# Performance work log

Measured on AMD Instinct MI355X. Metric: run time of the kernel, lower is better.

The kernel has to match this reference:

```python
import jax, jax.numpy as jnp
import numpy as np

PAD_Y = 16
PAD_X = 16


def setup_inputs() -> dict:
    key = jax.random.key(0)
    k1, k2, k3, k4 = jax.random.split(key, 4)
    B, NLAM, H, W = 4, 96, 256, 256
    KS = 15
    cube = jax.random.normal(k1, (B, NLAM, H, W), dtype=jnp.float32)
    # per-(ksequence, wavelength) dispersion shifts in pixels (a few px)
    dx = 3.0 * jax.random.normal(k2, (4, NLAM), dtype=jnp.float32)
    dy = 3.0 * jax.random.normal(k3, (4, NLAM), dtype=jnp.float32)
    psf = jax.random.uniform(k4, (KS, KS), dtype=jnp.float32)
    psf = psf / psf.sum()  # normalised PSF as in the original
    return {"cube": cube, "dx": dx, "dy": dy, "psf_kernel": psf}


def _forward(cube, dx, dy, psf_kernel):
    B, n_lam, H, W = cube.shape
    H_out, W_out = H + 2 * PAD_Y, W + 2 * PAD_X
    padded = jnp.pad(cube, ((0, 0), (0, 0), (PAD_Y, PAD_Y), (PAD_X, PAD_X)))
    yy, xx = jnp.meshgrid(jnp.arange(H_out, dtype=cube.dtype),
                          jnp.arange(W_out, dtype=cube.dtype), indexing="ij")

    def shift_one(img_b, d_x, d_y):
        # img_b: (B, H_out, W_out); output[y,x] = input[y-dy, x-dx], bilinear,
        # zeros outside (matches grid_sample padding_mode='zeros', align_corners=True)
        coords = jnp.stack([yy - d_y, xx - d_x])  # (2, H_out, W_out)
        return jax.vmap(lambda im: jax.scipy.ndimage.map_coordinates(
            im, coords, order=1, mode="constant", cval=0.0))(img_b)

    def per_k(dxk, dyk):
        # vmap over wavelengths -> (n_lam, B, H_out, W_out); accumulate over lambda
        shifted = jax.vmap(shift_one, in_axes=(1, 0, 0))(padded, dxk, dyk)
        return shifted.sum(0)  # (B, H_out, W_out)

    acc = jax.vmap(per_k)(dx, dy)            # (4, B, H_out, W_out)
    acc = jnp.transpose(acc, (1, 0, 2, 3))   # (B, 4, H_out, W_out)

    # PSF conv (same kernel every channel); conv is linear so conv(sum) == sum(conv)
    ks = psf_kernel.shape[-1]
    p = ks // 2
    x = acc.reshape(B * 4, 1, H_out, W_out)
    kern = psf_kernel.reshape(1, 1, ks, ks)
    out = jax.lax.conv_general_dilated(
        x, kern, window_strides=(1, 1), padding=[(p, p), (p, p)],
        dimension_numbers=("NCHW", "OIHW", "NCHW"))
    return out.reshape(B, 4, H_out, W_out)


def reference(cube, dx, dy, psf_kernel):
    return _forward(cube, dx, dy, psf_kernel)
```

## Files before the change

### kernel.cpp

```cpp
#include <hip/hip_runtime.h>

#define BB 4
#define NLAM 96
#define HH 256
#define WW 256
#define HO 288
#define WO 288
#define NK 4
#define KS 15
#define PADK 7

#define ACC_N ((size_t)BB * NK * HO * WO)

#define SP 104
#define NQ 7
#define TILE_Q (NQ * 256)

typedef float f4a __attribute__((ext_vector_type(4)));
typedef float f8v __attribute__((ext_vector_type(8), aligned(16)));

__global__ __launch_bounds__(384) void params_k(const float* __restrict__ dx,
                                                const float* __restrict__ dy,
                                                float4* __restrict__ pw,
                                                int2* __restrict__ po,
                                                int4* __restrict__ gmm,
                                                float* __restrict__ zp) {
    __shared__ int sox[384], soy[384];
    const int i = threadIdx.x;
    if (i < 32) zp[i] = 0.0f;
    const float sx = -dx[i] - 16.0f;
    const float sy = -dy[i] - 16.0f;
    const float fx = floorf(sx), fy = floorf(sy);
    const int ox = (int)fx, oy = (int)fy;
    po[i] = make_int2(ox, oy);
    pw[i] = make_float4(1.0f - (sx - fx), sx - fx, 1.0f - (sy - fy), sy - fy);
    sox[i] = ox; soy[i] = oy;
    __syncthreads();
    if (i < 64) {
        int mnx = sox[i], mxx = mnx, mny = soy[i], mxy = mny;
        for (int j = i + 64; j < 384; j += 64) {
            mnx = min(mnx, sox[j]); mxx = max(mxx, sox[j]);
            mny = min(mny, soy[j]); mxy = max(mxy, soy[j]);
        }
        for (int m = 32; m; m >>= 1) {
            mnx = min(mnx, __shfl_xor(mnx, m, 64));
            mxx = max(mxx, __shfl_xor(mxx, m, 64));
            mny = min(mny, __shfl_xor(mny, m, 64));
            mxy = max(mxy, __shfl_xor(mxy, m, 64));
        }
        if (i == 0) *gmm = make_int4(mnx, mxx, mny, mxy);
    }
}

#define HORW(P)                                                          \
    {                                                                    \
        f4a h0  = {vb0[P], vb0[(P)+1], vb0[(P)+2], vb0[(P)+3]};          \
        f4a h0s = {vb0[(P)+1], vb0[(P)+2], vb0[(P)+3], vb0[(P)+4]};      \
        f4a h1  = {vb1[P], vb1[(P)+1], vb1[(P)+2], vb1[(P)+3]};          \
        f4a h1s = {vb1[(P)+1], vb1[(P)+2], vb1[(P)+3], vb1[(P)+4]};      \
        a[k][0] += w.x * h0 + w.y * h0s;                                 \
        a[k][1] += w.x * h1 + w.y * h1s;                                 \
    }

__global__ __launch_bounds__(256, 2) void shift_accum(
        const float* __restrict__ cube,
        const float4* __restrict__ pw,
        const int2* __restrict__ po,
        const int4* __restrict__ gmm,
        const float* __restrict__ zp,
        float* __restrict__ part,
        int S, int chunk) {
    __shared__ __align__(16) float tile[TILE_Q * 4 + 8];
    const int zc  = blockIdx.z;
    const int b   = zc / S;
    const int c   = zc - b * S;
    const int tx0 = blockIdx.x * 64;
    const int ty0 = blockIdx.y * 32;
    const int tx  = threadIdx.x, ty = threadIdx.y;
    const int x   = tx0 + tx * 4;
    const int y   = ty0 + ty * 2;
    const int tid = ty * 16 + tx;
    const float* __restrict__ cb = cube + (size_t)b * NLAM * HH * WW;

    const int4 mm = *gmm;
    const int spanX = mm.y - mm.x;
    const int spanY = mm.w - mm.z;
    const bool lds_ok = (spanX <= 32) && (spanY <= 31);

    f4a a[NK][2];
#pragma unroll
    for (int k = 0; k < NK; ++k) { a[k][0] = (f4a)0.f; a[k][1] = (f4a)0.f; }

    const int l0 = min(NLAM, c * chunk);
    const int l1 = min(NLAM, l0 + chunk);

    if (lds_ok) {
        const int row0 = ty0 + mm.z;
        const int col0 = (tx0 + mm.x) & ~3;
        const int R    = spanY + 34;
        const int Rq   = R * 26;
        const int dx0  = tx0 - col0;
        const int tb0  = (ty * 2 - mm.z) * SP + tx * 4 + dx0;
        const int ldsq0 = tid & 192;
        const char* zpc = (const char*)zp;

        int goffB[NQ];
        int fm = 0;
        int pf = 0;
#pragma unroll
        for (int s = 0; s < NQ; ++s) {
            const int q  = tid + s * 256;
            const bool inR = q < Rq;
            const int r  = q / 26;
            const int qi = q - r * 26;
            const int gy = row0 + r;
            const int gc = col0 + qi * 4;
            const bool rowOK = (unsigned)gy < (unsigned)HH;
            const bool fullQ = inR && rowOK && gc >= 0 && gc <= WW - 4;
            const bool partQ = inR && rowOK && !fullQ && (gc + 3 >= 0) && (gc < WW);
            goffB[s] = (gy * WW + gc) * 4;
            if (fullQ) fm |= 1 << s;
            if (partQ) pf |= 1 << s;
        }

        for (int lam = l0; lam < l1; ++lam) {
            const char* __restrict__ ib = (const char*)(cb + lam * (HH * WW));
#pragma unroll
            for (int s = 0; s < NQ; ++s) {
                if (s * 256 < Rq) {
                    const char* src = ((fm >> s) & 1) ? (ib + goffB[s]) : zpc;
                    __builtin_amdgcn_global_load_lds(
                        (const __attribute__((address_space(1))) unsigned int*)src,
                        (__attribute__((address_space(3))) unsigned int*)
                            (tile + (s * 256 + ldsq0) * 4),
                        16, 0, 0);
                }
            }
            if (pf) {
                asm volatile("s_waitcnt vmcnt(0)" ::: "memory");
#pragma unroll
                for (int s = 0; s < NQ; ++s) {
                    if (pf & (1 << s)) {
                        const int q  = tid + s * 256;
                        const int r  = q / 26;
                        const int qi = q - r * 26;
                        const int gy = row0 + r;
                        const int gc = col0 + qi * 4;
                        const float* rp = (const float*)ib + gy * WW;
                        const int la = r * SP + qi * 4;
#pragma unroll
                        for (int e = 0; e < 4; ++e)
                            tile[la + e] = ((unsigned)(gc + e) < (unsigned)WW)
                                               ? rp[gc + e] : 0.0f;
                    }
                }
            }
            __syncthreads();
#pragma unroll
            for (int k = 0; k < NK; ++k) {
                const int2 o = po[k * NLAM + lam];
                const float4 w = pw[k * NLAM + lam];
                const int bidx = tb0 + o.y * SP + o.x;
                const int p = __builtin_amdgcn_readfirstlane(bidx & 3);
                const float* ta = tile + (bidx & ~3);
                const f8v R0 = *(const f8v*)ta;
                const f8v R1 = *(const f8v*)(ta + SP);
                const f8v R2 = *(const f8v*)(ta + 2 * SP);
                const f8v vb0 = w.z * R0 + w.w * R1;
                const f8v vb1 = w.z * R1 + w.w * R2;
                switch (p) {
                    case 0:  HORW(0); break;
                    case 1:  HORW(1); break;
                    case 2:  HORW(2); break;
                    default: HORW(3); break;
                }
            }
            __syncthreads();
        }
    } else {
        for (int lam = l0; lam < l1; ++lam) {
            const float* __restrict__ img = cb + lam * (HH * WW);
#pragma unroll
            for (int k = 0; k < NK; ++k) {
                const int i_ = k * NLAM + lam;
                const int2 o = po[i_]; const float4 w = pw[i_];
#pragma unroll
                for (int j = 0; j < 2; ++j) {
                    const int iy = y + j + o.y;
                    const int ix = x + o.x;
                    const int cy0 = min(max(iy, 0), HH - 1);
                    const int cy1 = min(max(iy + 1, 0), HH - 1);
                    const float my0 = ((unsigned)iy       < (unsigned)HH) ? w.z : 0.0f;
                    const float my1 = ((unsigned)(iy + 1) < (unsigned)HH) ? w.w : 0.0f;
                    const float* r0p = img + cy0 * WW;
                    const float* r1p = img + cy1 * WW;
                    float rb[5];
#pragma unroll
                    for (int cc = 0; cc < 5; ++cc) {
                        const int cx = min(max(ix + cc, 0), WW - 1);
                        const float m = ((unsigned)(ix + cc) < (unsigned)WW) ? 1.0f : 0.0f;
                        rb[cc] = m * (my0 * r0p[cx] + my1 * r1p[cx]);
                    }
                    f4a d;
                    d.x = w.x * rb[0] + w.y * rb[1];
                    d.y = w.x * rb[1] + w.y * rb[2];
                    d.z = w.x * rb[2] + w.y * rb[3];
                    d.w = w.x * rb[3] + w.y * rb[4];
                    a[k][j] += d;
                }
            }
        }
    }

    if (x < WO) {
        const size_t hw = (size_t)HO * WO;
        float* pa = part + (size_t)c * ACC_N + ((size_t)(b * NK) * HO + y) * WO + x;
#pragma unroll
        for (int k = 0; k < NK; ++k) {
            *(f4a*)(pa + (size_t)k * hw)      = a[k][0];
            *(f4a*)(pa + (size_t)k * hw + WO) = a[k][1];
        }
    }
}

template <int S>
__global__ __launch_bounds__(256) void reduce_k(float* __restrict__ part) {
    const size_t i = ((size_t)blockIdx.x * 256 + threadIdx.x) * 4;
    f4a acc = *(const f4a*)(part + i);
#pragma unroll
    for (int cc = 1; cc < S; ++cc)
        acc += *(const f4a*)(part + (size_t)cc * ACC_N + i);
    *(f4a*)(part + i) = acc;
}

#define CPX 112
#define CROWS 30
#define CTILE_N (CROWS * CPX)
#define NQC 5

__global__ __launch_bounds__(192) void conv_psf(const float* __restrict__ part,
                                                const float* __restrict__ psf,
                                                float* __restrict__ out) {
    __shared__ __align__(16) float tilec[CTILE_N + 16];
    __shared__ __align__(16) float spsf[KS][16];
    const int bk  = blockIdx.z;
    const int gx0 = blockIdx.x * 96 - 8;
    const int gy0 = blockIdx.y * 16 - PADK;
    const float* __restrict__ ap = part + (size_t)bk * HO * WO;

    const int tid = threadIdx.y * 24 + threadIdx.x;
    for (int i = tid; i < KS * 16; i += 192) {
        const int r = i >> 4, cc2 = i & 15;
        spsf[r][cc2] = (cc2 < KS) ? psf[r * KS + cc2] : 0.0f;
    }

#pragma unroll
    for (int s = 0; s < NQC; ++s) {
        const int q  = tid + s * 192;
        const bool inR = q < CROWS * 28;
        const int r  = q / 28;
        const int qi = q - r * 28;
        const int gy = gy0 + r;
        const int gx = gx0 + qi * 4;
        const bool rowOK = (unsigned)gy < (unsigned)HO;
        const int gyc = min(max(gy, 0), HO - 1);
        const int goffB = (gyc * WO + gx) * 4;
        const int laddr = inR ? (r * CPX + qi * 4) : CTILE_N;
        f4a m;
#pragma unroll
        for (int e = 0; e < 4; ++e)
            m[e] = (inR && rowOK && (unsigned)(gx + e) < (unsigned)WO) ? 1.0f : 0.0f;
        f4a v = *(const f4a*)((const char*)ap + goffB);
        *(f4a*)(tilec + laddr) = v * m;
    }
    __syncthreads();

    const int x0 = threadIdx.x * 4;
    const int y0 = threadIdx.y * 2;
    f4a o0 = (f4a)0.f, o1 = (f4a)0.f;
    f4a prev0, prev1, prev2, prev3;

#pragma unroll
    for (int rr = 0; rr < 16; ++rr) {
        const float* rp = &tilec[(y0 + rr) * CPX + x0];
        float row[20];
#pragma unroll
        for (int q = 0; q < 5; ++q) {
            f4a v = *(const f4a*)(rp + 4 * q);
            row[4 * q]     = v.x; row[4 * q + 1] = v.y;
            row[4 * q + 2] = v.z; row[4 * q + 3] = v.w;
        }

        f4a c0, c1, c2, c3;
        if (rr < 15) {
            c0 = *(const f4a*)&spsf[rr][0];
            c1 = *(const f4a*)&spsf[rr][4];
            c2 = *(const f4a*)&spsf[rr][8];
            c3 = *(const f4a*)&spsf[rr][12];
        }
        if (rr < 15) {
#pragma unroll
            for (int kx = 0; kx < KS; ++kx) {
                const float wv = (kx < 4) ? c0[kx] : (kx < 8) ? c1[kx - 4]
                               : (kx < 12) ? c2[kx - 8] : c3[kx - 12];
                f4a rv = {row[kx + 1], row[kx + 2], row[kx + 3], row[kx + 4]};
                o0 += wv * rv;
            }
        }
        if (rr >= 1) {
#pragma unroll
            for (int kx = 0; kx < KS; ++kx) {
                const float wv = (kx < 4) ? prev0[kx] : (kx < 8) ? prev1[kx - 4]
                               : (kx < 12) ? prev2[kx - 8] : prev3[kx - 12];
                f4a rv = {row[kx + 1], row[kx + 2], row[kx + 3], row[kx + 4]};
                o1 += wv * rv;
            }
        }
        prev0 = c0; prev1 = c1; prev2 = c2; prev3 = c3;
    }

    const int xo = blockIdx.x * 96 + x0;
    const int yo = blockIdx.y * 16 + y0;
    float* op = out + ((size_t)bk * HO + yo) * WO + xo;
    *(f4a*)op        = o0;
    *(f4a*)(op + WO) = o1;
}

extern "C" void kernel_launch(void* const* d_in, const int* in_sizes, int n_in,
                              void* d_out, int out_size, void* d_ws, size_t ws_size,
                              hipStream_t stream) {
    const float* cube = (const float*)d_in[0];
    const float* dx   = (const float*)d_in[1];
    const float* dy   = (const float*)d_in[2];
    const float* psf  = (const float*)d_in[3];
    float* out = (float*)d_out;

    const size_t ACCB   = ACC_N * sizeof(float);
    const size_t tables = 384 * sizeof(float4) + 384 * sizeof(int2) + sizeof(int4);

    int S = 1;
    for (int cand : {12, 8, 6, 4, 3, 2}) {
        if (ws_size >= 128 + (size_t)cand * ACCB + tables + 4096) { S = cand; break; }
    }
    const int chunk = (NLAM + S - 1) / S;

    float* zp   = (float*)d_ws;
    float* part = (float*)((char*)d_ws + 128);
    char*  tb   = (char*)part + (size_t)S * ACCB;
    float4* pw  = (float4*)tb;
    int2*   po  = (int2*)(tb + 384 * sizeof(float4));
    int4*   gmm = (int4*)(tb + 384 * sizeof(float4) + 384 * sizeof(int2));

    params_k<<<1, 384, 0, stream>>>(dx, dy, pw, po, gmm, zp);

    dim3 b1(16, 16);
    dim3 g1((WO + 63) / 64, HO / 32, BB * S);
    shift_accum<<<g1, b1, 0, stream>>>(cube, pw, po, gmm, zp, part, S, chunk);

    const int rblocks = (int)(ACC_N / 4 / 256);
    switch (S) {
        case 12: reduce_k<12><<<rblocks, 256, 0, stream>>>(part); break;
        case 8:  reduce_k<8><<<rblocks, 256, 0, stream>>>(part); break;
        case 6:  reduce_k<6><<<rblocks, 256, 0, stream>>>(part); break;
        case 4:  reduce_k<4><<<rblocks, 256, 0, stream>>>(part); break;
        case 3:  reduce_k<3><<<rblocks, 256, 0, stream>>>(part); break;
        case 2:  reduce_k<2><<<rblocks, 256, 0, stream>>>(part); break;
        default: break;
    }

    dim3 b2(24, 8);
    dim3 g2(WO / 96, HO / 16, BB * NK);
    conv_psf<<<g2, b2, 0, stream>>>(part, psf, out);
}
```

Baseline: 206.1 us.

## Replace split-lambda partial buffers and reduce kernel with float atomics

Each lambda-chunk block now atomically adds its accumulated values into a single zeroed accumulation buffer. This drops the S-way partial buffers and the separate reduce kernel, cutting the extra global write/read traffic and one launch. It adds a memset of the accumulator and 12-way atomic contention per output element using scalar unsafeAtomicAdd. The chunk count is fixed at 12 instead of depending on workspace size, and block index decoding now places the batch in the low bits.

```diff
diff --git a/kernel.cpp b/kernel.cpp
--- a/kernel.cpp
+++ b/kernel.cpp
@@ -16,6 +16,8 @@
 #define NQ 7
 #define TILE_Q (NQ * 256)
 
+#define NCH 12
+
 typedef float f4a __attribute__((ext_vector_type(4)));
 typedef float f8v __attribute__((ext_vector_type(8), aligned(16)));
 
@@ -23,11 +25,9 @@
                                                 const float* __restrict__ dy,
                                                 float4* __restrict__ pw,
                                                 int2* __restrict__ po,
-                                                int4* __restrict__ gmm,
-                                                float* __restrict__ zp) {
+                                                int4* __restrict__ gmm) {
     __shared__ int sox[384], soy[384];
     const int i = threadIdx.x;
-    if (i < 32) zp[i] = 0.0f;
     const float sx = -dx[i] - 16.0f;
     const float sy = -dy[i] - 16.0f;
     const float fx = floorf(sx), fy = floorf(sy);
@@ -68,12 +68,12 @@
         const int2* __restrict__ po,
         const int4* __restrict__ gmm,
         const float* __restrict__ zp,
-        float* __restrict__ part,
-        int S, int chunk) {
+        float* __restrict__ acc,
+        int chunk) {
     __shared__ __align__(16) float tile[TILE_Q * 4 + 8];
     const int zc  = blockIdx.z;
-    const int b   = zc / S;
-    const int c   = zc - b * S;
+    const int b   = zc & (BB - 1);
+    const int c   = zc >> 2;
     const int tx0 = blockIdx.x * 64;
     const int ty0 = blockIdx.y * 32;
     const int tx  = threadIdx.x, ty = threadIdx.y;
@@ -214,23 +214,18 @@
 
     if (x < WO) {
         const size_t hw = (size_t)HO * WO;
-        float* pa = part + (size_t)c * ACC_N + ((size_t)(b * NK) * HO + y) * WO + x;
+        float* pa = acc + ((size_t)(b * NK) * HO + y) * WO + x;
 #pragma unroll
         for (int k = 0; k < NK; ++k) {
-            *(f4a*)(pa + (size_t)k * hw)      = a[k][0];
-            *(f4a*)(pa + (size_t)k * hw + WO) = a[k][1];
-        }
-    }
-}
-
-template <int S>
-__global__ __launch_bounds__(256) void reduce_k(float* __restrict__ part) {
-    const size_t i = ((size_t)blockIdx.x * 256 + threadIdx.x) * 4;
-    f4a acc = *(const f4a*)(part + i);
-#pragma unroll
-    for (int cc = 1; cc < S; ++cc)
-        acc += *(const f4a*)(part + (size_t)cc * ACC_N + i);
-    *(f4a*)(part + i) = acc;
+#pragma unroll
+            for (int j = 0; j < 2; ++j) {
+                float* p4 = pa + (size_t)k * hw + j * WO;
+#pragma unroll
+                for (int e = 0; e < 4; ++e)
+                    unsafeAtomicAdd(p4 + e, a[k][j][e]);
+            }
+        }
+    }
 }
 
 #define CPX 112
@@ -238,7 +233,7 @@
 #define CTILE_N (CROWS * CPX)
 #define NQC 5
 
-__global__ __launch_bounds__(192) void conv_psf(const float* __restrict__ part,
+__global__ __launch_bounds__(192) void conv_psf(const float* __restrict__ acc,
                                                 const float* __restrict__ psf,
                                                 float* __restrict__ out) {
     __shared__ __align__(16) float tilec[CTILE_N + 16];
@@ -246,7 +241,7 @@
     const int bk  = blockIdx.z;
     const int gx0 = blockIdx.x * 96 - 8;
     const int gy0 = blockIdx.y * 16 - PADK;
-    const float* __restrict__ ap = part + (size_t)bk * HO * WO;
+    const float* __restrict__ ap = acc + (size_t)bk * HO * WO;
 
     const int tid = threadIdx.y * 24 + threadIdx.x;
     for (int i = tid; i < KS * 16; i += 192) {
@@ -335,40 +330,25 @@
     const float* psf  = (const float*)d_in[3];
     float* out = (float*)d_out;
 
-    const size_t ACCB   = ACC_N * sizeof(float);
-    const size_t tables = 384 * sizeof(float4) + 384 * sizeof(int2) + sizeof(int4);
-
-    int S = 1;
-    for (int cand : {12, 8, 6, 4, 3, 2}) {
-        if (ws_size >= 128 + (size_t)cand * ACCB + tables + 4096) { S = cand; break; }
-    }
-    const int chunk = (NLAM + S - 1) / S;
+    const size_t ACCB = ACC_N * sizeof(float);
+    const int chunk = (NLAM + NCH - 1) / NCH;
 
     float* zp   = (float*)d_ws;
-    float* part = (float*)((char*)d_ws + 128);
-    char*  tb   = (char*)part + (size_t)S * ACCB;
+    float* acc  = (float*)((char*)d_ws + 128);
+    char*  tb   = (char*)d_ws + 128 + ACCB + 64;
     float4* pw  = (float4*)tb;
     int2*   po  = (int2*)(tb + 384 * sizeof(float4));
     int4*   gmm = (int4*)(tb + 384 * sizeof(float4) + 384 * sizeof(int2));
 
-    params_k<<<1, 384, 0, stream>>>(dx, dy, pw, po, gmm, zp);
+    hipMemsetAsync(d_ws, 0, 128 + ACCB + 64, stream);
+
+    params_k<<<1, 384, 0, stream>>>(dx, dy, pw, po, gmm);
 
     dim3 b1(16, 16);
-    dim3 g1((WO + 63) / 64, HO / 32, BB * S);
-    shift_accum<<<g1, b1, 0, stream>>>(cube, pw, po, gmm, zp, part, S, chunk);
-
-    const int rblocks = (int)(ACC_N / 4 / 256);
-    switch (S) {
-        case 12: reduce_k<12><<<rblocks, 256, 0, stream>>>(part); break;
-        case 8:  reduce_k<8><<<rblocks, 256, 0, stream>>>(part); break;
-        case 6:  reduce_k<6><<<rblocks, 256, 0, stream>>>(part); break;
-        case 4:  reduce_k<4><<<rblocks, 256, 0, stream>>>(part); break;
-        case 3:  reduce_k<3><<<rblocks, 256, 0, stream>>>(part); break;
-        case 2:  reduce_k<2><<<rblocks, 256, 0, stream>>>(part); break;
-        default: break;
-    }
+    dim3 g1((WO + 63) / 64, HO / 32, NCH * BB);
+    shift_accum<<<g1, b1, 0, stream>>>(cube, pw, po, gmm, zp, acc, chunk);
 
     dim3 b2(24, 8);
     dim3 g2(WO / 96, HO / 16, BB * NK);
-    conv_psf<<<g2, b2, 0, stream>>>(part, psf, out);
+    conv_psf<<<g2, b2, 0, stream>>>(acc, psf, out);
 }
```

Measured after the change: 357.4 us. 1.73x slower.

## Prefetch next wavelength tile into registers instead of direct-to-LDS loads

Applied to the files above, without the earlier changes.

Replaces the per-wavelength global_load_lds fill, and its wait-for-completion stall, with a register double-buffer. The next wavelength's quads are loaded into VGPRs while the current tile is gathered, then written to LDS between two barriers. Out-of-range quads are handled with clamped addresses and a multiply by a 0/1 mask instead of a zero-page pointer and a scalar fallback path. The gather now uses 4-wide reads plus a few scalar reads in place of 8-wide vectors. The cost is higher register pressure (seven f4a prefetch registers) under launch_bounds(256,2), plus an explicit VGPR-to-LDS store per wavelength.

```diff
diff --git a/kernel.cpp b/kernel.cpp
--- a/kernel.cpp
+++ b/kernel.cpp
@@ -14,20 +14,18 @@
 
 #define SP 104
 #define NQ 7
-#define TILE_Q (NQ * 256)
+#define TILE_N (65 * SP)
+#define SDUMMY TILE_N
 
 typedef float f4a __attribute__((ext_vector_type(4)));
-typedef float f8v __attribute__((ext_vector_type(8), aligned(16)));
 
 __global__ __launch_bounds__(384) void params_k(const float* __restrict__ dx,
                                                 const float* __restrict__ dy,
                                                 float4* __restrict__ pw,
                                                 int2* __restrict__ po,
-                                                int4* __restrict__ gmm,
-                                                float* __restrict__ zp) {
+                                                int4* __restrict__ gmm) {
     __shared__ int sox[384], soy[384];
     const int i = threadIdx.x;
-    if (i < 32) zp[i] = 0.0f;
     const float sx = -dx[i] - 16.0f;
     const float sy = -dy[i] - 16.0f;
     const float fx = floorf(sx), fy = floorf(sy);
@@ -52,14 +50,66 @@
     }
 }
 
-#define HORW(P)                                                          \
-    {                                                                    \
-        f4a h0  = {vb0[P], vb0[(P)+1], vb0[(P)+2], vb0[(P)+3]};          \
-        f4a h0s = {vb0[(P)+1], vb0[(P)+2], vb0[(P)+3], vb0[(P)+4]};      \
-        f4a h1  = {vb1[P], vb1[(P)+1], vb1[(P)+2], vb1[(P)+3]};          \
-        f4a h1s = {vb1[(P)+1], vb1[(P)+2], vb1[(P)+3], vb1[(P)+4]};      \
-        a[k][0] += w.x * h0 + w.y * h0s;                                 \
-        a[k][1] += w.x * h1 + w.y * h1s;                                 \
+#define BLEND5(T00,T01,T02,T03,T04, T10,T11,T12,T13,T14, T20,T21,T22,T23,T24) \
+    {                                                                         \
+        f4a r0v = {T00, T01, T02, T03};                                       \
+        f4a r1v = {T10, T11, T12, T13};                                       \
+        f4a r2v = {T20, T21, T22, T23};                                       \
+        f4a vb0 = w.z * r0v + w.w * r1v;                                      \
+        f4a vb1 = w.z * r1v + w.w * r2v;                                      \
+        const float e0 = w.z * (T04) + w.w * (T14);                           \
+        const float e1 = w.z * (T14) + w.w * (T24);                           \
+        f4a s0 = {vb0.y, vb0.z, vb0.w, e0};                                   \
+        f4a s1 = {vb1.y, vb1.z, vb1.w, e1};                                   \
+        a[k][0] += w.x * vb0 + w.y * s0;                                      \
+        a[k][1] += w.x * vb1 + w.y * s1;                                      \
+    }
+
+#define GATHER_ALL_K(LAM)                                                        \
+    _Pragma("unroll")                                                            \
+    for (int k = 0; k < NK; ++k) {                                               \
+        const int2 o = po[k * NLAM + (LAM)];                                     \
+        const float4 w = pw[k * NLAM + (LAM)];                                   \
+        const int bidx = tb0 + o.y * SP + o.x;                                   \
+        const int p = __builtin_amdgcn_readfirstlane(bidx & 3);                  \
+        const float* ta = tile + (bidx & ~3);                                    \
+        const float* tbp = ta + SP;                                             \
+        const float* tcp = ta + 2 * SP;                                         \
+        switch (p) {                                                             \
+            case 0: {                                                            \
+                f4a A = *(const f4a*)ta, B = *(const f4a*)tbp, C = *(const f4a*)tcp; \
+                const float xa = ta[4], xb = tbp[4], xc = tcp[4];                \
+                BLEND5(A.x, A.y, A.z, A.w, xa,                                   \
+                       B.x, B.y, B.z, B.w, xb,                                   \
+                       C.x, C.y, C.z, C.w, xc)                                   \
+            } break;                                                             \
+            case 1: {                                                            \
+                f4a A = *(const f4a*)ta, B = *(const f4a*)tbp, C = *(const f4a*)tcp; \
+                const float xa0 = ta[4], xa1 = ta[5];                            \
+                const float xb0 = tbp[4], xb1 = tbp[5];                          \
+                const float xc0 = tcp[4], xc1 = tcp[5];                          \
+                BLEND5(A.y, A.z, A.w, xa0, xa1,                                  \
+                       B.y, B.z, B.w, xb0, xb1,                                  \
+                       C.y, C.z, C.w, xc0, xc1)                                  \
+            } break;                                                             \
+            case 2: {                                                            \
+                f4a A = *(const f4a*)ta, B = *(const f4a*)tbp, C = *(const f4a*)tcp; \
+                const float xa0 = ta[4], xa1 = ta[5], xa2 = ta[6];               \
+                const float xb0 = tbp[4], xb1 = tbp[5], xb2 = tbp[6];            \
+                const float xc0 = tcp[4], xc1 = tcp[5], xc2 = tcp[6];            \
+                BLEND5(A.z, A.w, xa0, xa1, xa2,                                  \
+                       B.z, B.w, xb0, xb1, xb2,                                  \
+                       C.z, C.w, xc0, xc1, xc2)                                  \
+            } break;                                                             \
+            default: {                                                           \
+                f4a A = *(const f4a*)ta, A2 = *(const f4a*)(ta + 4);             \
+                f4a B = *(const f4a*)tbp, B2 = *(const f4a*)(tbp + 4);           \
+                f4a C = *(const f4a*)tcp, C2 = *(const f4a*)(tcp + 4);           \
+                BLEND5(A.w, A2.x, A2.y, A2.z, A2.w,                              \
+                       B.w, B2.x, B2.y, B2.z, B2.w,                              \
+                       C.w, C2.x, C2.y, C2.z, C2.w)                              \
+            } break;                                                             \
+        }                                                                        \
     }
 
 __global__ __launch_bounds__(256, 2) void shift_accum(
@@ -67,10 +117,9 @@
         const float4* __restrict__ pw,
         const int2* __restrict__ po,
         const int4* __restrict__ gmm,
-        const float* __restrict__ zp,
         float* __restrict__ part,
         int S, int chunk) {
-    __shared__ __align__(16) float tile[TILE_Q * 4 + 8];
+    __shared__ __align__(16) float tile[TILE_N + 16];
     const int zc  = blockIdx.z;
     const int b   = zc / S;
     const int c   = zc - b * S;
@@ -101,12 +150,10 @@
         const int Rq   = R * 26;
         const int dx0  = tx0 - col0;
         const int tb0  = (ty * 2 - mm.z) * SP + tx * 4 + dx0;
-        const int ldsq0 = tid & 192;
-        const char* zpc = (const char*)zp;
-
-        int goffB[NQ];
-        int fm = 0;
-        int pf = 0;
+
+        int   goffB[NQ];
+        int   la[NQ];
+        float mf[NQ];
 #pragma unroll
         for (int s = 0; s < NQ; ++s) {
             const int q  = tid + s * 256;
@@ -117,65 +164,41 @@
             const int gc = col0 + qi * 4;
             const bool rowOK = (unsigned)gy < (unsigned)HH;
             const bool fullQ = inR && rowOK && gc >= 0 && gc <= WW - 4;
-            const bool partQ = inR && rowOK && !fullQ && (gc + 3 >= 0) && (gc < WW);
-            goffB[s] = (gy * WW + gc) * 4;
-            if (fullQ) fm |= 1 << s;
-            if (partQ) pf |= 1 << s;
+            const int gyc = min(max(gy, 0), HH - 1);
+            const int gcc = min(max(gc, 0), WW - 4);
+            goffB[s] = (gyc * WW + gcc) * 4;
+            mf[s]    = fullQ ? 1.0f : 0.0f;
+            la[s]    = inR ? (r * SP + qi * 4) : SDUMMY;
+        }
+
+        f4a v[NQ];
+        {
+            const char* ib0 = (const char*)(cb + l0 * (HH * WW));
+#pragma unroll
+            for (int s = 0; s < NQ; ++s)
+                v[s] = *(const f4a*)(ib0 + goffB[s]);
+#pragma unroll
+            for (int s = 0; s < NQ; ++s)
+                *(f4a*)(tile + la[s]) = v[s] * mf[s];
+            __syncthreads();
         }
 
         for (int lam = l0; lam < l1; ++lam) {
-            const char* __restrict__ ib = (const char*)(cb + lam * (HH * WW));
-#pragma unroll
-            for (int s = 0; s < NQ; ++s) {
-                if (s * 256 < Rq) {
-                    const char* src = ((fm >> s) & 1) ? (ib + goffB[s]) : zpc;
-                    __builtin_amdgcn_global_load_lds(
-                        (const __attribute__((address_space(1))) unsigned int*)src,
-                        (__attribute__((address_space(3))) unsigned int*)
-                            (tile + (s * 256 + ldsq0) * 4),
-                        16, 0, 0);
-                }
-            }
-            if (pf) {
-                asm volatile("s_waitcnt vmcnt(0)" ::: "memory");
-#pragma unroll
-                for (int s = 0; s < NQ; ++s) {
-                    if (pf & (1 << s)) {
-                        const int q  = tid + s * 256;
-                        const int r  = q / 26;
-                        const int qi = q - r * 26;
-                        const int gy = row0 + r;
-                        const int gc = col0 + qi * 4;
-                        const float* rp = (const float*)ib + gy * WW;
-                        const int la = r * SP + qi * 4;
-#pragma unroll
-                        for (int e = 0; e < 4; ++e)
-                            tile[la + e] = ((unsigned)(gc + e) < (unsigned)WW)
-                                               ? rp[gc + e] : 0.0f;
-                    }
-                }
-            }
-            __syncthreads();
-#pragma unroll
-            for (int k = 0; k < NK; ++k) {
-                const int2 o = po[k * NLAM + lam];
-                const float4 w = pw[k * NLAM + lam];
-                const int bidx = tb0 + o.y * SP + o.x;
-                const int p = __builtin_amdgcn_readfirstlane(bidx & 3);
-                const float* ta = tile + (bidx & ~3);
-                const f8v R0 = *(const f8v*)ta;
-                const f8v R1 = *(const f8v*)(ta + SP);
-                const f8v R2 = *(const f8v*)(ta + 2 * SP);
-                const f8v vb0 = w.z * R0 + w.w * R1;
-                const f8v vb1 = w.z * R1 + w.w * R2;
-                switch (p) {
-                    case 0:  HORW(0); break;
-                    case 1:  HORW(1); break;
-                    case 2:  HORW(2); break;
-                    default: HORW(3); break;
-                }
-            }
-            __syncthreads();
+            const bool hasNext = (lam + 1 < l1);
+            if (hasNext) {
+                const char* ibn = (const char*)(cb + (lam + 1) * (HH * WW));
+#pragma unroll
+                for (int s = 0; s < NQ; ++s)
+                    v[s] = *(const f4a*)(ibn + goffB[s]);
+            }
+            GATHER_ALL_K(lam)
+            if (hasNext) {
+                __syncthreads();
+#pragma unroll
+                for (int s = 0; s < NQ; ++s)
+                    *(f4a*)(tile + la[s]) = v[s] * mf[s];
+                __syncthreads();
+            }
         }
     } else {
         for (int lam = l0; lam < l1; ++lam) {
@@ -344,18 +367,17 @@
     }
     const int chunk = (NLAM + S - 1) / S;
 
-    float* zp   = (float*)d_ws;
     float* part = (float*)((char*)d_ws + 128);
     char*  tb   = (char*)part + (size_t)S * ACCB;
     float4* pw  = (float4*)tb;
     int2*   po  = (int2*)(tb + 384 * sizeof(float4));
     int4*   gmm = (int4*)(tb + 384 * sizeof(float4) + 384 * sizeof(int2));
 
-    params_k<<<1, 384, 0, stream>>>(dx, dy, pw, po, gmm, zp);
+    params_k<<<1, 384, 0, stream>>>(dx, dy, pw, po, gmm);
 
     dim3 b1(16, 16);
     dim3 g1((WO + 63) / 64, HO / 32, BB * S);
-    shift_accum<<<g1, b1, 0, stream>>>(cube, pw, po, gmm, zp, part, S, chunk);
+    shift_accum<<<g1, b1, 0, stream>>>(cube, pw, po, gmm, part, S, chunk);
 
     const int rblocks = (int)(ACC_N / 4 / 256);
     switch (S) {
```

Result: slower. 218.6 us (+6.1%).
